# Optimization experiments

Hardware: AMD Instinct MI355X
Metric: run time of the kernel (lower is better)

The kernel has to match this reference:

```python
import jax, jax.numpy as jnp
import numpy as np

EMBED = 768
HEADS = 12
HEAD_DIM = EMBED // HEADS
HIDDEN = 4 * EMBED
EPS = 1e-5


def _layernorm(x, w, b):
    mu = jnp.mean(x, axis=-1, keepdims=True)
    var = jnp.mean(jnp.square(x - mu), axis=-1, keepdims=True)
    return (x - mu) * jax.lax.rsqrt(var + EPS) * w + b


def setup_inputs() -> dict:
    key = jax.random.key(0)
    ks = jax.random.split(key, 12)
    s = 0.02
    return {
        "x": jax.random.normal(ks[0], (2, 2048, EMBED), dtype=jnp.float32),
        "ln1_w": jnp.ones((EMBED,), jnp.float32),
        "ln1_b": jnp.zeros((EMBED,), jnp.float32),
        "qkv_w": jax.random.normal(ks[1], (3 * EMBED, EMBED), jnp.float32) * s,
        "qkv_b": jnp.zeros((3 * EMBED,), jnp.float32),
        "proj_w": jax.random.normal(ks[2], (EMBED, EMBED), jnp.float32) * s,
        "proj_b": jnp.zeros((EMBED,), jnp.float32),
        "ln2_w": jnp.ones((EMBED,), jnp.float32),
        "ln2_b": jnp.zeros((EMBED,), jnp.float32),
        "fc1_w": jax.random.normal(ks[3], (HIDDEN, EMBED), jnp.float32) * s,
        "fc1_b": jnp.zeros((HIDDEN,), jnp.float32),
        "fc2_w": jax.random.normal(ks[4], (EMBED, HIDDEN), jnp.float32) * s,
        "fc2_b": jnp.zeros((EMBED,), jnp.float32),
    }


def reference(x, ln1_w, ln1_b, qkv_w, qkv_b, proj_w, proj_b,
              ln2_w, ln2_b, fc1_w, fc1_b, fc2_w, fc2_b):
    B, N, C = x.shape
    scale = float(HEAD_DIM) ** 0.5  # NOTE: module MULTIPLIES by sqrt(head_dim)

    # --- attention branch ---
    h = _layernorm(x, ln1_w, ln1_b)
    qkv = h @ qkv_w.T + qkv_b                     # [B,N,3C]
    qkv = qkv.reshape(B, N, 3, HEADS, HEAD_DIM)
    q = qkv[:, :, 0].transpose(0, 2, 1, 3)        # [B,H,N,D]
    k = qkv[:, :, 1].transpose(0, 2, 1, 3)
    v = qkv[:, :, 2].transpose(0, 2, 1, 3)
    attn = jnp.einsum('bhnd,bhmd->bhnm', q, k) * scale
    attn = jax.nn.softmax(attn, axis=-1)
    o = jnp.einsum('bhnm,bhmd->bhnd', attn, v)    # [B,H,N,D]
    o = o.transpose(0, 2, 1, 3).reshape(B, N, C)
    x = x + (o @ proj_w.T + proj_b)

    # --- MLP branch ---
    h = _layernorm(x, ln2_w, ln2_b)
    h = jax.nn.gelu(h @ fc1_w.T + fc1_b, approximate=False)
    x = x + (h @ fc2_w.T + fc2_b)
    return x
```

## Files before the change

kernel.cpp:

```cpp
#include <hip/hip_runtime.h>
#include <hip/hip_bf16.h>

typedef __attribute__((ext_vector_type(8))) short short8;
typedef __attribute__((ext_vector_type(4))) float f32x4;
typedef __attribute__((ext_vector_type(4))) int i32x4;

__device__ inline unsigned short f2bs(float f) {
  union { float f; unsigned u; } v; v.f = f;
  unsigned r = v.u + 0x7fff + ((v.u >> 16) & 1);
  return (unsigned short)(r >> 16);
}

__device__ inline float bs2f(unsigned short u) {
  union { unsigned u; float f; } c; c.u = (unsigned)u << 16; return c.f;
}

__device__ inline unsigned pkbf(float a, float b) {
  __hip_bfloat162 h = __float22bfloat162_rn(float2{a, b});
  union { __hip_bfloat162 h; unsigned u; } c; c.h = h;
  return c.u;
}

__device__ inline float exp2v(float x) {
  float r; asm("v_exp_f32 %0, %1" : "=v"(r) : "v"(x)); return r;
}

__device__ inline float max3f(float a, float b, float c) {
  return fmaxf(fmaxf(a, b), c);
}

__device__ inline void gload16(const void* g, void* l) {
  __builtin_amdgcn_global_load_lds((const __attribute__((address_space(1))) void*)g,
                                   (__attribute__((address_space(3))) void*)l,
                                   16, 0, 0);
}

__global__ __launch_bounds__(256)
void cvt_all(const float* __restrict__ s0, const float* __restrict__ s1,
             const float* __restrict__ s2, const float* __restrict__ s3,
             unsigned short* __restrict__ d0, unsigned short* __restrict__ d1,
             unsigned short* __restrict__ d2, unsigned short* __restrict__ d3)
{
  size_t i = (size_t)blockIdx.x * 256 + threadIdx.x;
  const float* src; unsigned short* dst;
  if (i < 442368) { src = s0; dst = d0; }
  else if (i < 589824) { src = s1; dst = d1; i -= 442368; }
  else if (i < 1179648) { src = s2; dst = d2; i -= 589824; }
  else { src = s3; dst = d3; i -= 1179648; }
  float4 v = ((const float4*)src)[i];
  ushort4 o;
  o.x = f2bs(v.x); o.y = f2bs(v.y); o.z = f2bs(v.z); o.w = f2bs(v.w);
  ((ushort4*)dst)[i] = o;
}

__global__ __launch_bounds__(256)
void ln_kernel(const float* __restrict__ x, const float* __restrict__ w,
               const float* __restrict__ bsh, unsigned short* __restrict__ out)
{
  const int row = blockIdx.x;
  const float* xr = x + (size_t)row * 768;
  float v[3];
  float s = 0.f, sq = 0.f;
#pragma unroll
  for (int i = 0; i < 3; ++i) {
    v[i] = xr[threadIdx.x + i * 256];
    s += v[i]; sq += v[i] * v[i];
  }
#pragma unroll
  for (int d = 1; d < 64; d <<= 1) {
    s  += __shfl_xor(s, d, 64);
    sq += __shfl_xor(sq, d, 64);
  }
  __shared__ float ss[4], ssq[4];
  const int wv = threadIdx.x >> 6;
  if ((threadIdx.x & 63) == 0) { ss[wv] = s; ssq[wv] = sq; }
  __syncthreads();
  s  = ss[0] + ss[1] + ss[2] + ss[3];
  sq = ssq[0] + ssq[1] + ssq[2] + ssq[3];
  const float mu = s * (1.0f / 768.0f);
  const float var = sq * (1.0f / 768.0f) - mu * mu;
  const float rstd = rsqrtf(var + 1e-5f);
#pragma unroll
  for (int i = 0; i < 3; ++i) {
    const int c = threadIdx.x + i * 256;
    out[(size_t)row * 768 + c] = f2bs((v[i] - mu) * rstd * w[c] + bsh[c]);
  }
}

__global__ __launch_bounds__(256)
void reduce_ln2(const unsigned short* __restrict__ p, const float* __restrict__ bias,
                const float* __restrict__ resid, const float* __restrict__ lw,
                const float* __restrict__ lb, float* __restrict__ x2,
                unsigned short* __restrict__ h)
{
  const size_t MN = 4096ull * 768;
  const int row = blockIdx.x;
  const size_t r0 = (size_t)row * 768;
  float v[3];
  float s = 0.f, sq = 0.f;
#pragma unroll
  for (int i = 0; i < 3; ++i) {
    const int c = threadIdx.x + i * 256;
    const float a = bs2f(p[r0 + c]) + bs2f(p[MN + r0 + c]) + bias[c] + resid[r0 + c];
    x2[r0 + c] = a;
    v[i] = a; s += a; sq += a * a;
  }
#pragma unroll
  for (int d = 1; d < 64; d <<= 1) {
    s  += __shfl_xor(s, d, 64);
    sq += __shfl_xor(sq, d, 64);
  }
  __shared__ float ss[4], ssq[4];
  const int wv = threadIdx.x >> 6;
  if ((threadIdx.x & 63) == 0) { ss[wv] = s; ssq[wv] = sq; }
  __syncthreads();
  s  = ss[0] + ss[1] + ss[2] + ss[3];
  sq = ssq[0] + ssq[1] + ssq[2] + ssq[3];
  const float mu = s * (1.0f / 768.0f);
  const float var = sq * (1.0f / 768.0f) - mu * mu;
  const float rstd = rsqrtf(var + 1e-5f);
#pragma unroll
  for (int i = 0; i < 3; ++i) {
    const int c = threadIdx.x + i * 256;
    h[r0 + c] = f2bs((v[i] - mu) * rstd * lw[c] + lb[c]);
  }
}

template<int S>
__global__ __launch_bounds__(256)
void reduce_k(const unsigned short* __restrict__ p, const float* __restrict__ bias,
              const float* __restrict__ resid, float* __restrict__ out)
{
  const size_t MN = 4096ull * 768;
  const size_t i = ((size_t)blockIdx.x * 256 + threadIdx.x) * 4;
  float ax = 0.f, ay = 0.f, az = 0.f, aw = 0.f;
#pragma unroll
  for (int s = 0; s < S; ++s) {
    ushort4 b = *(const ushort4*)(p + s * MN + i);
    ax += bs2f(b.x); ay += bs2f(b.y); az += bs2f(b.z); aw += bs2f(b.w);
  }
  const int col = (int)(i % 768);
  float4 bb = *(const float4*)(bias + col);
  float4 rr = *(const float4*)(resid + i);
  float4 r;
  r.x = ax + bb.x + rr.x; r.y = ay + bb.y + rr.y;
  r.z = az + bb.z + rr.z; r.w = aw + bb.w + rr.w;
  *(float4*)(out + i) = r;
}

template<int EPI>
__global__ __launch_bounds__(256, 3)
void gemm_nt(const unsigned short* __restrict__ A,
             const unsigned short* __restrict__ Bw,
             const float* __restrict__ bias,
             const float* __restrict__ resid,
             void* __restrict__ out0, void* __restrict__ out1, void* __restrict__ out2,
             int M, int N, int Kslice, int Kstride)
{
  __shared__ __align__(16) unsigned short As[3][128 * 32];
  __shared__ __align__(16) unsigned short Bs[3][128 * 32];
  const int tid = threadIdx.x;
  const int lane = tid & 63;
  const int w = tid >> 6;
  const int wr = w >> 1, wc = w & 1;
  const int l15 = lane & 15, g = lane >> 4;

  const int nwg = gridDim.x * gridDim.y;
  const int hw = blockIdx.y * gridDim.x + blockIdx.x;
  const int virt = (hw & 7) * (nwg >> 3) + (hw >> 3);
  const int m0 = (virt / gridDim.x) * 128;
  const int n0 = (virt % gridDim.x) * 128;
  const int kbase = blockIdx.z * Kslice;

  f32x4 acc[4][4];
#pragma unroll
  for (int m = 0; m < 4; ++m)
#pragma unroll
    for (int n = 0; n < 4; ++n)
      acc[m][n] = (f32x4){0.f, 0.f, 0.f, 0.f};

  auto stage = [&](int buf, int k0) {
#pragma unroll
    for (int i = 0; i < 2; ++i) {
      const int f = tid + i * 256;
      const int row = f >> 2, c8 = f & 3;
      const int sc = c8 ^ (row & 3);
      gload16(A  + (size_t)(m0 + row) * Kstride + kbase + k0 + sc * 8, (char*)&As[buf][0] + f * 16);
      gload16(Bw + (size_t)(n0 + row) * Kstride + kbase + k0 + sc * 8, (char*)&Bs[buf][0] + f * 16);
    }
  };

  const int NT = Kslice >> 5;
  stage(0, 0);
  stage(1, 32);

  for (int t = 0; t < NT; ++t) {
    const int buf = t % 3;
    if (t + 1 < NT) {
      asm volatile("s_waitcnt vmcnt(4)" ::: "memory");
    } else {
      asm volatile("s_waitcnt vmcnt(0)" ::: "memory");
    }
    __builtin_amdgcn_s_barrier();
    asm volatile("" ::: "memory");
    if (t + 2 < NT) stage((t + 2) % 3, (t + 2) * 32);

    short8 af[4], bfr[4];
#pragma unroll
    for (int m = 0; m < 4; ++m) {
      const int r = wr * 64 + m * 16 + l15;
      af[m] = *(const short8*)((const char*)&As[buf][0] + ((size_t)r * 32 + (g ^ (r & 3)) * 8) * 2);
    }
#pragma unroll
    for (int n = 0; n < 4; ++n) {
      const int r = wc * 64 + n * 16 + l15;
      bfr[n] = *(const short8*)((const char*)&Bs[buf][0] + ((size_t)r * 32 + (g ^ (r & 3)) * 8) * 2);
    }
#pragma unroll
    for (int m = 0; m < 4; ++m)
#pragma unroll
      for (int n = 0; n < 4; ++n)
        acc[m][n] = __builtin_amdgcn_mfma_f32_16x16x32_bf16(af[m], bfr[n], acc[m][n], 0, 0, 0);
    asm volatile("" ::: "memory");
  }

#pragma unroll
  for (int m = 0; m < 4; ++m) {
    const int gmBase = m0 + wr * 64 + m * 16 + g * 4;
#pragma unroll
    for (int n = 0; n < 4; ++n) {
      const int gn = n0 + wc * 64 + n * 16 + l15;
      const float bval = (EPI == 4) ? 0.0f : bias[gn];
      float vj[4];
#pragma unroll
      for (int j = 0; j < 4; ++j) vj[j] = acc[m][n][j] + bval;
      if (EPI == 0) {
        const int three = gn / 768;
        const int hh = (gn % 768) >> 6;
        const int d = gn & 63;
        const int bb = gmBase >> 11, t = gmBase & 2047;
        if (three == 2) {
          ushort4 pk;
          pk.x = f2bs(vj[0]); pk.y = f2bs(vj[1]); pk.z = f2bs(vj[2]); pk.w = f2bs(vj[3]);
          const int kt = t & 63;
          const size_t pos = ((((size_t)(bb * 12 + hh) * 32 + (t >> 6)) * 8 + (d >> 4) * 2 + (kt >> 5)) * 64
                              + ((kt >> 2) & 3) * 16 + (d & 15)) * 8 + ((kt >> 4) & 1) * 4;
          *(ushort4*)((unsigned short*)out2 + pos) = pk;
        } else if (three == 1) {
          unsigned short* dst = (unsigned short*)out1;
          const int gt = t >> 6;
          const int kt0 = t & 63;
          const int fb = d >> 5;
          const int ge = (d >> 3) & 3;
          const int e = d & 7;
          const size_t base9 = ((size_t)(bb * 12 + hh) * 32 + gt) * 8;
#pragma unroll
          for (int j = 0; j < 4; ++j) {
            const int kt = kt0 + j;
            const size_t pos = (base9 + (kt >> 4) * 2 + fb) * 512 + (ge * 16 + (kt & 15)) * 8 + e;
            dst[pos] = f2bs(vj[j]);
          }
        } else {
          unsigned short* dst = (unsigned short*)out0;
#pragma unroll
          for (int j = 0; j < 4; ++j) {
            dst[(((size_t)bb * 12 + hh) * 2048 + (t + j)) * 64 + d] = f2bs(vj[j] * 11.5415603f);
          }
        }
      } else if (EPI == 1 || EPI == 3) {
#pragma unroll
        for (int j = 0; j < 4; ++j) {
          const int gm = gmBase + j;
          ((float*)out0)[(size_t)gm * N + gn] = vj[j] + resid[(size_t)gm * N + gn];
        }
      } else if (EPI == 2) {
#pragma unroll
        for (int j = 0; j < 4; ++j) {
          const int gm = gmBase + j;
          const float vv = vj[j];
          const float u = vv * (1.0f + 0.044715f * vv * vv);
          const float E = exp2v(2.0f * 0.7978845608f * 1.4426950409f * u);
          const float ge = vv - vv / (1.0f + E);
          ((unsigned short*)out0)[(size_t)gm * N + gn] = f2bs(ge);
        }
      } else {
        unsigned short* po = (unsigned short*)out0 + (size_t)blockIdx.z * M * N;
#pragma unroll
        for (int j = 0; j < 4; ++j) {
          const int gm = gmBase + j;
          po[(size_t)gm * N + gn] = f2bs(vj[j]);
        }
      }
    }
  }
}

template<int SPLIT>
__global__ __launch_bounds__(256, 6)
void attn_fwd(const unsigned short* __restrict__ Q,
              const unsigned short* __restrict__ Kf,
              const unsigned short* __restrict__ Vf,
              unsigned short* __restrict__ O,
              unsigned short* __restrict__ Op, float* __restrict__ Mb, float* __restrict__ Lb)
{
  __shared__ __align__(1024) unsigned short Ks[4096];
  __shared__ __align__(1024) unsigned short Vs[2][4096];
  const int tid = threadIdx.x, lane = tid & 63, w = tid >> 6;
  const int l15 = lane & 15, g = lane >> 4;

  const int hw = blockIdx.y * gridDim.x + blockIdx.x;
  const int virt = (hw & 7) * 96 + (hw >> 3);
  const int qblk = virt & 31;
  const int bh = virt >> 5;
  const int b = bh / 12, h = bh % 12;
  const int q0 = qblk * 64;
  const int half = SPLIT ? blockIdx.z : 0;
  const int NT = SPLIT ? 16 : 32;
  const int T0 = half * 16;
  const unsigned short* Qb = Q  + (size_t)bh * 2048 * 64;
  const unsigned short* Kb = Kf + (size_t)bh * 2048 * 64;
  const unsigned short* Vb = Vf + (size_t)bh * 2048 * 64;

  const int qr = q0 + w * 16 + l15;
  short8 qf[2];
  qf[0] = *(const short8*)(Qb + (size_t)qr * 64 + g * 8);
  qf[1] = *(const short8*)(Qb + (size_t)qr * 64 + 32 + g * 8);

  float m_run = -1e30f, l_part = 0.f;
  f32x4 o_acc[4];
#pragma unroll
  for (int dc = 0; dc < 4; ++dc) o_acc[dc] = (f32x4){0.f, 0.f, 0.f, 0.f};

  auto stageK = [&](int gt) {
#pragma unroll
    for (int i = 0; i < 2; ++i) {
      const int chunk = tid + i * 256;
      gload16(Kb + (size_t)gt * 4096 + chunk * 8, (char*)&Ks[0] + chunk * 16);
    }
  };
  auto stageV = [&](int buf, int gt) {
#pragma unroll
    for (int i = 0; i < 2; ++i) {
      const int chunk = tid + i * 256;
      gload16(Vb + (size_t)gt * 4096 + chunk * 8, (char*)&Vs[buf][0] + chunk * 16);
    }
  };

  stageK(T0);
  stageV(0, T0);

  for (int t = 0; t < NT; ++t) {
    const int vbuf = t & 1;
    asm volatile("s_waitcnt vmcnt(0)" ::: "memory");
    __builtin_amdgcn_s_barrier();
    asm volatile("" ::: "memory");
    if (t + 1 < NT) stageV(vbuf ^ 1, T0 + t + 1);

    f32x4 s2[4];
#pragma unroll
    for (int n = 0; n < 4; ++n) s2[n] = (f32x4){0.f, 0.f, 0.f, 0.f};
    __builtin_amdgcn_s_setprio(1);
#pragma unroll
    for (int n = 0; n < 4; ++n) {
      short8 kf0 = *(const short8*)(&Ks[(n * 2 + 0) * 512 + lane * 8]);
      short8 kf1 = *(const short8*)(&Ks[(n * 2 + 1) * 512 + lane * 8]);
      s2[n] = __builtin_amdgcn_mfma_f32_16x16x32_bf16(kf0, qf[0], s2[n], 0, 0, 0);
      s2[n] = __builtin_amdgcn_mfma_f32_16x16x32_bf16(kf1, qf[1], s2[n], 0, 0, 0);
    }
    __builtin_amdgcn_s_setprio(0);

    asm volatile("" ::: "memory");
    __builtin_amdgcn_s_barrier();
    asm volatile("" ::: "memory");
    if (t + 1 < NT) stageK(T0 + t + 1);

    float mx = max3f(max3f(s2[0][0], s2[0][1], s2[0][2]),
                     max3f(s2[0][3], s2[1][0], s2[1][1]),
                     max3f(s2[1][2], s2[1][3], s2[2][0]));
    mx = max3f(mx, max3f(s2[2][1], s2[2][2], s2[2][3]),
                   max3f(s2[3][0], s2[3][1], fmaxf(s2[3][2], s2[3][3])));
    mx = fmaxf(mx, __shfl_xor(mx, 16, 64));
    mx = fmaxf(mx, __shfl_xor(mx, 32, 64));
    if (__any(mx > m_run + 8.0f)) {
      const float mn = fmaxf(m_run, mx);
      const float alpha = exp2v(m_run - mn);
      m_run = mn;
      l_part *= alpha;
#pragma unroll
      for (int j = 0; j < 4; ++j) {
        const float aB = __shfl(alpha, (lane & 48) | (g * 4 + j), 64);
#pragma unroll
        for (int dc = 0; dc < 4; ++dc) o_acc[dc][j] *= aB;
      }
    }
    float e[4][4];
    float rs = 0.f;
#pragma unroll
    for (int n = 0; n < 4; ++n)
#pragma unroll
      for (int j = 0; j < 4; ++j) {
        e[n][j] = exp2v(s2[n][j] - m_run);
        rs += e[n][j];
      }
    l_part += rs;

    unsigned pw[2][4];
#pragma unroll
    for (int kc = 0; kc < 2; ++kc) {
      pw[kc][0] = pkbf(e[2 * kc][0],     e[2 * kc][1]);
      pw[kc][1] = pkbf(e[2 * kc][2],     e[2 * kc][3]);
      pw[kc][2] = pkbf(e[2 * kc + 1][0], e[2 * kc + 1][1]);
      pw[kc][3] = pkbf(e[2 * kc + 1][2], e[2 * kc + 1][3]);
    }

    const char* vsb = (const char*)&Vs[vbuf][0];
    __builtin_amdgcn_s_setprio(1);
#pragma unroll
    for (int kc = 0; kc < 2; ++kc) {
      i32x4 pt; pt.x = (int)pw[kc][0]; pt.y = (int)pw[kc][1]; pt.z = (int)pw[kc][2]; pt.w = (int)pw[kc][3];
      short8 pf = *(short8*)&pt;
#pragma unroll
      for (int dc = 0; dc < 4; ++dc) {
        short8 vfr = *(const short8*)(vsb + (((dc * 2 + kc) * 64 + lane) * 16));
        o_acc[dc] = __builtin_amdgcn_mfma_f32_16x16x32_bf16(pf, vfr, o_acc[dc], 0, 0, 0);
      }
    }
    __builtin_amdgcn_s_setprio(0);
    asm volatile("" ::: "memory");
  }

  l_part += __shfl_xor(l_part, 16, 64);
  l_part += __shfl_xor(l_part, 32, 64);
  if (SPLIT) {
    const int rowBase = (half * 24 + bh) * 2048;
    if (g == 0) {
      const int qm = q0 + w * 16 + l15;
      Mb[rowBase + qm] = m_run;
      Lb[rowBase + qm] = l_part;
    }
#pragma unroll
    for (int j = 0; j < 4; ++j) {
      const int row = q0 + w * 16 + g * 4 + j;
#pragma unroll
      for (int dc = 0; dc < 4; ++dc)
        Op[(size_t)(rowBase + row) * 64 + dc * 16 + l15] = f2bs(o_acc[dc][j]);
    }
  } else {
#pragma unroll
    for (int j = 0; j < 4; ++j) {
      const float lB = __shfl(l_part, (lane & 48) | (g * 4 + j), 64);
      const float inv = 1.0f / lB;
      const int qrow = q0 + w * 16 + g * 4 + j;
#pragma unroll
      for (int dc = 0; dc < 4; ++dc)
        O[((size_t)b * 2048 + qrow) * 768 + h * 64 + dc * 16 + l15] = f2bs(o_acc[dc][j] * inv);
    }
  }
}

__global__ __launch_bounds__(256)
void attn_combine(const unsigned short* __restrict__ Op, const float* __restrict__ Mb,
                  const float* __restrict__ Lb, unsigned short* __restrict__ O)
{
  const int idx = blockIdx.x * 256 + threadIdx.x;
  const int e4 = idx * 4;
  const int row = e4 >> 6;
  const int d0 = e4 & 63;
  const float m1 = Mb[row], m2 = Mb[49152 + row];
  const float l1 = Lb[row], l2 = Lb[49152 + row];
  const float mm = fmaxf(m1, m2);
  const float w1 = exp2v(m1 - mm), w2 = exp2v(m2 - mm);
  const float inv = 1.0f / (l1 * w1 + l2 * w2);
  ushort4 a1 = *(const ushort4*)(Op + (size_t)row * 64 + d0);
  ushort4 a2 = *(const ushort4*)(Op + 49152ull * 64 + (size_t)row * 64 + d0);
  ushort4 r;
  r.x = f2bs((bs2f(a1.x) * w1 + bs2f(a2.x) * w2) * inv);
  r.y = f2bs((bs2f(a1.y) * w1 + bs2f(a2.y) * w2) * inv);
  r.z = f2bs((bs2f(a1.z) * w1 + bs2f(a2.z) * w2) * inv);
  r.w = f2bs((bs2f(a1.w) * w1 + bs2f(a2.w) * w2) * inv);
  const int bh = row >> 11, q = row & 2047;
  const int b = bh / 12, hh = bh % 12;
  *(ushort4*)(O + ((size_t)(b * 2048 + q)) * 768 + hh * 64 + d0) = r;
}

extern "C" void kernel_launch(void* const* d_in, const int* in_sizes, int n_in,
                              void* d_out, int out_size, void* d_ws, size_t ws_size,
                              hipStream_t stream)
{
  const float* x      = (const float*)d_in[0];
  const float* ln1_w  = (const float*)d_in[1];
  const float* ln1_b  = (const float*)d_in[2];
  const float* qkv_w  = (const float*)d_in[3];
  const float* qkv_b  = (const float*)d_in[4];
  const float* proj_w = (const float*)d_in[5];
  const float* proj_b = (const float*)d_in[6];
  const float* ln2_w  = (const float*)d_in[7];
  const float* ln2_b  = (const float*)d_in[8];
  const float* fc1_w  = (const float*)d_in[9];
  const float* fc1_b  = (const float*)d_in[10];
  const float* fc2_w  = (const float*)d_in[11];
  const float* fc2_b  = (const float*)d_in[12];

  char* base = (char*)d_ws;
  size_t off = 0;
  auto take = [&](size_t bytes) {
    void* r = base + off;
    off = (off + bytes + 255) & ~(size_t)255;
    return r;
  };
  unsigned short* wq = (unsigned short*)take(2304ull * 768 * 2);
  unsigned short* wp = (unsigned short*)take(768ull * 768 * 2);
  unsigned short* w1 = (unsigned short*)take(3072ull * 768 * 2);
  unsigned short* w2 = (unsigned short*)take(768ull * 3072 * 2);
  unsigned short* h  = (unsigned short*)take(4096ull * 768 * 2);
  float* x2          = (float*)take(4096ull * 768 * 4);
  char* big          = (char*)take(4096ull * 3072 * 2);
  unsigned short* Qb = (unsigned short*)big;
  unsigned short* Kb = (unsigned short*)(big + 4096ull * 768 * 2);
  unsigned short* Vb = (unsigned short*)(big + 2ull * 4096 * 768 * 2);
  unsigned short* a2 = (unsigned short*)big;
  unsigned short* part = (unsigned short*)take(4ull * 4096 * 768 * 2);
  float* Mb_         = (float*)take(2ull * 49152 * 4);
  float* Lb_         = (float*)take(2ull * 49152 * 4);
  const bool can_split = off <= ws_size;

  cvt_all<<<6912, 256, 0, stream>>>(qkv_w, proj_w, fc1_w, fc2_w, wq, wp, w1, w2);

  ln_kernel<<<4096, 256, 0, stream>>>(x, ln1_w, ln1_b, h);
  gemm_nt<0><<<dim3(18, 32), 256, 0, stream>>>(h, wq, qkv_b, nullptr, Qb, Kb, Vb, 4096, 2304, 768, 768);

  if (can_split) {
    attn_fwd<1><<<dim3(32, 24, 2), 256, 0, stream>>>(Qb, Kb, Vb, nullptr, part, Mb_, Lb_);
    attn_combine<<<3072, 256, 0, stream>>>(part, Mb_, Lb_, h);
  } else {
    attn_fwd<0><<<dim3(32, 24), 256, 0, stream>>>(Qb, Kb, Vb, h, nullptr, nullptr, nullptr);
  }

  if (can_split) {
    gemm_nt<4><<<dim3(6, 32, 2), 256, 0, stream>>>(h, wp, nullptr, nullptr, part, nullptr, nullptr, 4096, 768, 384, 768);
    reduce_ln2<<<4096, 256, 0, stream>>>(part, proj_b, x, ln2_w, ln2_b, x2, h);
  } else {
    gemm_nt<1><<<dim3(6, 32), 256, 0, stream>>>(h, wp, proj_b, x, x2, nullptr, nullptr, 4096, 768, 768, 768);
    ln_kernel<<<4096, 256, 0, stream>>>(x2, ln2_w, ln2_b, h);
  }

  gemm_nt<2><<<dim3(24, 32), 256, 0, stream>>>(h, w1, fc1_b, nullptr, a2, nullptr, nullptr, 4096, 3072, 768, 768);

  if (can_split) {
    gemm_nt<4><<<dim3(6, 32, 4), 256, 0, stream>>>(a2, w2, nullptr, nullptr, part, nullptr, nullptr, 4096, 768, 768, 3072);
    reduce_k<4><<<3072, 256, 0, stream>>>(part, fc2_b, x2, (float*)d_out);
  } else {
    gemm_nt<3><<<dim3(6, 32), 256, 0, stream>>>(a2, w2, fc2_b, x2, d_out, nullptr, nullptr, 4096, 768, 3072, 3072);
  }
}
```

Before: 188.1 us.

## Process 128 query rows per attention block, split KV four ways, fuse prep

The attention kernel now has each wave handle two 16-row query groups (128 queries per block), so every K/V tile staged into LDS is reused by twice as many queries. The key range is split four ways instead of two, and the combine step merges four partial results. The weight conversion and first layernorm are merged into a single launch. This trades higher register pressure and a larger combine step for less LDS staging traffic and one fewer launch.

After: 241.9 us. 1.29x slower.

```diff
diff --git a/kernel.cpp b/kernel.cpp
--- a/kernel.cpp
+++ b/kernel.cpp
@@ -36,21 +36,54 @@
 }
 
 __global__ __launch_bounds__(256)
-void cvt_all(const float* __restrict__ s0, const float* __restrict__ s1,
-             const float* __restrict__ s2, const float* __restrict__ s3,
-             unsigned short* __restrict__ d0, unsigned short* __restrict__ d1,
-             unsigned short* __restrict__ d2, unsigned short* __restrict__ d3)
-{
-  size_t i = (size_t)blockIdx.x * 256 + threadIdx.x;
-  const float* src; unsigned short* dst;
-  if (i < 442368) { src = s0; dst = d0; }
-  else if (i < 589824) { src = s1; dst = d1; i -= 442368; }
-  else if (i < 1179648) { src = s2; dst = d2; i -= 589824; }
-  else { src = s3; dst = d3; i -= 1179648; }
-  float4 v = ((const float4*)src)[i];
-  ushort4 o;
-  o.x = f2bs(v.x); o.y = f2bs(v.y); o.z = f2bs(v.z); o.w = f2bs(v.w);
-  ((ushort4*)dst)[i] = o;
+void prep(const float* __restrict__ s0, const float* __restrict__ s1,
+          const float* __restrict__ s2, const float* __restrict__ s3,
+          unsigned short* __restrict__ d0, unsigned short* __restrict__ d1,
+          unsigned short* __restrict__ d2, unsigned short* __restrict__ d3,
+          const float* __restrict__ x, const float* __restrict__ lw,
+          const float* __restrict__ lb, unsigned short* __restrict__ out)
+{
+  if (blockIdx.x < 6912) {
+    size_t i = (size_t)blockIdx.x * 256 + threadIdx.x;
+    const float* src; unsigned short* dst;
+    if (i < 442368) { src = s0; dst = d0; }
+    else if (i < 589824) { src = s1; dst = d1; i -= 442368; }
+    else if (i < 1179648) { src = s2; dst = d2; i -= 589824; }
+    else { src = s3; dst = d3; i -= 1179648; }
+    float4 v = ((const float4*)src)[i];
+    ushort4 o;
+    o.x = f2bs(v.x); o.y = f2bs(v.y); o.z = f2bs(v.z); o.w = f2bs(v.w);
+    ((ushort4*)dst)[i] = o;
+    return;
+  }
+  const int row = blockIdx.x - 6912;
+  const float* xr = x + (size_t)row * 768;
+  float v[3];
+  float s = 0.f, sq = 0.f;
+#pragma unroll
+  for (int i = 0; i < 3; ++i) {
+    v[i] = xr[threadIdx.x + i * 256];
+    s += v[i]; sq += v[i] * v[i];
+  }
+#pragma unroll
+  for (int d = 1; d < 64; d <<= 1) {
+    s  += __shfl_xor(s, d, 64);
+    sq += __shfl_xor(sq, d, 64);
+  }
+  __shared__ float ss[4], ssq[4];
+  const int wv = threadIdx.x >> 6;
+  if ((threadIdx.x & 63) == 0) { ss[wv] = s; ssq[wv] = sq; }
+  __syncthreads();
+  s  = ss[0] + ss[1] + ss[2] + ss[3];
+  sq = ssq[0] + ssq[1] + ssq[2] + ssq[3];
+  const float mu = s * (1.0f / 768.0f);
+  const float var = sq * (1.0f / 768.0f) - mu * mu;
+  const float rstd = rsqrtf(var + 1e-5f);
+#pragma unroll
+  for (int i = 0; i < 3; ++i) {
+    const int c = threadIdx.x + i * 256;
+    out[(size_t)row * 768 + c] = f2bs((v[i] - mu) * rstd * lw[c] + lb[c]);
+  }
 }
 
 __global__ __launch_bounds__(256)
@@ -308,28 +341,32 @@
   const int tid = threadIdx.x, lane = tid & 63, w = tid >> 6;
   const int l15 = lane & 15, g = lane >> 4;
 
+  const int nwg = gridDim.x * gridDim.y;
   const int hw = blockIdx.y * gridDim.x + blockIdx.x;
-  const int virt = (hw & 7) * 96 + (hw >> 3);
-  const int qblk = virt & 31;
-  const int bh = virt >> 5;
+  const int virt = (hw & 7) * (nwg >> 3) + (hw >> 3);
+  const int qblk = virt & 15;
+  const int bh = virt >> 4;
   const int b = bh / 12, h = bh % 12;
-  const int q0 = qblk * 64;
-  const int half = SPLIT ? blockIdx.z : 0;
-  const int NT = SPLIT ? 16 : 32;
-  const int T0 = half * 16;
+  const int q0 = qblk * 128;
+  const int part = SPLIT ? blockIdx.z : 0;
+  const int NT = SPLIT ? 8 : 32;
+  const int T0 = part * 8;
   const unsigned short* Qb = Q  + (size_t)bh * 2048 * 64;
   const unsigned short* Kb = Kf + (size_t)bh * 2048 * 64;
   const unsigned short* Vb = Vf + (size_t)bh * 2048 * 64;
 
-  const int qr = q0 + w * 16 + l15;
-  short8 qf[2];
-  qf[0] = *(const short8*)(Qb + (size_t)qr * 64 + g * 8);
-  qf[1] = *(const short8*)(Qb + (size_t)qr * 64 + 32 + g * 8);
-
-  float m_run = -1e30f, l_part = 0.f;
-  f32x4 o_acc[4];
-#pragma unroll
-  for (int dc = 0; dc < 4; ++dc) o_acc[dc] = (f32x4){0.f, 0.f, 0.f, 0.f};
+  const int qra = q0 + w * 32 + l15;
+  const int qrb = qra + 16;
+  short8 qfa[2], qfb[2];
+  qfa[0] = *(const short8*)(Qb + (size_t)qra * 64 + g * 8);
+  qfa[1] = *(const short8*)(Qb + (size_t)qra * 64 + 32 + g * 8);
+  qfb[0] = *(const short8*)(Qb + (size_t)qrb * 64 + g * 8);
+  qfb[1] = *(const short8*)(Qb + (size_t)qrb * 64 + 32 + g * 8);
+
+  float m_a = -1e30f, l_a = 0.f, m_b = -1e30f, l_b = 0.f;
+  f32x4 oa[4], ob[4];
+#pragma unroll
+  for (int dc = 0; dc < 4; ++dc) { oa[dc] = (f32x4){0.f,0.f,0.f,0.f}; ob[dc] = (f32x4){0.f,0.f,0.f,0.f}; }
 
   auto stageK = [&](int gt) {
 #pragma unroll
@@ -364,8 +401,57 @@
     for (int n = 0; n < 4; ++n) {
       short8 kf0 = *(const short8*)(&Ks[(n * 2 + 0) * 512 + lane * 8]);
       short8 kf1 = *(const short8*)(&Ks[(n * 2 + 1) * 512 + lane * 8]);
-      s2[n] = __builtin_amdgcn_mfma_f32_16x16x32_bf16(kf0, qf[0], s2[n], 0, 0, 0);
-      s2[n] = __builtin_amdgcn_mfma_f32_16x16x32_bf16(kf1, qf[1], s2[n], 0, 0, 0);
+      s2[n] = __builtin_amdgcn_mfma_f32_16x16x32_bf16(kf0, qfa[0], s2[n], 0, 0, 0);
+      s2[n] = __builtin_amdgcn_mfma_f32_16x16x32_bf16(kf1, qfa[1], s2[n], 0, 0, 0);
+    }
+    __builtin_amdgcn_s_setprio(0);
+
+    unsigned pwa[2][4], pwb[2][4];
+    {
+      float mx = max3f(max3f(s2[0][0], s2[0][1], s2[0][2]),
+                       max3f(s2[0][3], s2[1][0], s2[1][1]),
+                       max3f(s2[1][2], s2[1][3], s2[2][0]));
+      mx = max3f(mx, max3f(s2[2][1], s2[2][2], s2[2][3]),
+                     max3f(s2[3][0], s2[3][1], fmaxf(s2[3][2], s2[3][3])));
+      mx = fmaxf(mx, __shfl_xor(mx, 16, 64));
+      mx = fmaxf(mx, __shfl_xor(mx, 32, 64));
+      if (__any(mx > m_a + 8.0f)) {
+        const float mn = fmaxf(m_a, mx);
+        const float alpha = exp2v(m_a - mn);
+        m_a = mn;
+        l_a *= alpha;
+#pragma unroll
+        for (int j = 0; j < 4; ++j) {
+          const float aB = __shfl(alpha, (lane & 48) | (g * 4 + j), 64);
+#pragma unroll
+          for (int dc = 0; dc < 4; ++dc) oa[dc][j] *= aB;
+        }
+      }
+      float rs = 0.f;
+#pragma unroll
+      for (int kc = 0; kc < 2; ++kc) {
+        float e0, e1;
+        e0 = exp2v(s2[2*kc][0] - m_a);   e1 = exp2v(s2[2*kc][1] - m_a);
+        rs += e0 + e1; pwa[kc][0] = pkbf(e0, e1);
+        e0 = exp2v(s2[2*kc][2] - m_a);   e1 = exp2v(s2[2*kc][3] - m_a);
+        rs += e0 + e1; pwa[kc][1] = pkbf(e0, e1);
+        e0 = exp2v(s2[2*kc+1][0] - m_a); e1 = exp2v(s2[2*kc+1][1] - m_a);
+        rs += e0 + e1; pwa[kc][2] = pkbf(e0, e1);
+        e0 = exp2v(s2[2*kc+1][2] - m_a); e1 = exp2v(s2[2*kc+1][3] - m_a);
+        rs += e0 + e1; pwa[kc][3] = pkbf(e0, e1);
+      }
+      l_a += rs;
+    }
+
+#pragma unroll
+    for (int n = 0; n < 4; ++n) s2[n] = (f32x4){0.f, 0.f, 0.f, 0.f};
+    __builtin_amdgcn_s_setprio(1);
+#pragma unroll
+    for (int n = 0; n < 4; ++n) {
+      short8 kf0 = *(const short8*)(&Ks[(n * 2 + 0) * 512 + lane * 8]);
+      short8 kf1 = *(const short8*)(&Ks[(n * 2 + 1) * 512 + lane * 8]);
+      s2[n] = __builtin_amdgcn_mfma_f32_16x16x32_bf16(kf0, qfb[0], s2[n], 0, 0, 0);
+      s2[n] = __builtin_amdgcn_mfma_f32_16x16x32_bf16(kf1, qfb[1], s2[n], 0, 0, 0);
     }
     __builtin_amdgcn_s_setprio(0);
 
@@ -374,86 +460,94 @@
     asm volatile("" ::: "memory");
     if (t + 1 < NT) stageK(T0 + t + 1);
 
-    float mx = max3f(max3f(s2[0][0], s2[0][1], s2[0][2]),
-                     max3f(s2[0][3], s2[1][0], s2[1][1]),
-                     max3f(s2[1][2], s2[1][3], s2[2][0]));
-    mx = max3f(mx, max3f(s2[2][1], s2[2][2], s2[2][3]),
-                   max3f(s2[3][0], s2[3][1], fmaxf(s2[3][2], s2[3][3])));
-    mx = fmaxf(mx, __shfl_xor(mx, 16, 64));
-    mx = fmaxf(mx, __shfl_xor(mx, 32, 64));
-    if (__any(mx > m_run + 8.0f)) {
-      const float mn = fmaxf(m_run, mx);
-      const float alpha = exp2v(m_run - mn);
-      m_run = mn;
-      l_part *= alpha;
-#pragma unroll
-      for (int j = 0; j < 4; ++j) {
-        const float aB = __shfl(alpha, (lane & 48) | (g * 4 + j), 64);
-#pragma unroll
-        for (int dc = 0; dc < 4; ++dc) o_acc[dc][j] *= aB;
-      }
-    }
-    float e[4][4];
-    float rs = 0.f;
-#pragma unroll
-    for (int n = 0; n < 4; ++n)
-#pragma unroll
-      for (int j = 0; j < 4; ++j) {
-        e[n][j] = exp2v(s2[n][j] - m_run);
-        rs += e[n][j];
-      }
-    l_part += rs;
-
-    unsigned pw[2][4];
-#pragma unroll
-    for (int kc = 0; kc < 2; ++kc) {
-      pw[kc][0] = pkbf(e[2 * kc][0],     e[2 * kc][1]);
-      pw[kc][1] = pkbf(e[2 * kc][2],     e[2 * kc][3]);
-      pw[kc][2] = pkbf(e[2 * kc + 1][0], e[2 * kc + 1][1]);
-      pw[kc][3] = pkbf(e[2 * kc + 1][2], e[2 * kc + 1][3]);
+    {
+      float mx = max3f(max3f(s2[0][0], s2[0][1], s2[0][2]),
+                       max3f(s2[0][3], s2[1][0], s2[1][1]),
+                       max3f(s2[1][2], s2[1][3], s2[2][0]));
+      mx = max3f(mx, max3f(s2[2][1], s2[2][2], s2[2][3]),
+                     max3f(s2[3][0], s2[3][1], fmaxf(s2[3][2], s2[3][3])));
+      mx = fmaxf(mx, __shfl_xor(mx, 16, 64));
+      mx = fmaxf(mx, __shfl_xor(mx, 32, 64));
+      if (__any(mx > m_b + 8.0f)) {
+        const float mn = fmaxf(m_b, mx);
+        const float alpha = exp2v(m_b - mn);
+        m_b = mn;
+        l_b *= alpha;
+#pragma unroll
+        for (int j = 0; j < 4; ++j) {
+          const float aB = __shfl(alpha, (lane & 48) | (g * 4 + j), 64);
+#pragma unroll
+          for (int dc = 0; dc < 4; ++dc) ob[dc][j] *= aB;
+        }
+      }
+      float rs = 0.f;
+#pragma unroll
+      for (int kc = 0; kc < 2; ++kc) {
+        float e0, e1;
+        e0 = exp2v(s2[2*kc][0] - m_b);   e1 = exp2v(s2[2*kc][1] - m_b);
+        rs += e0 + e1; pwb[kc][0] = pkbf(e0, e1);
+        e0 = exp2v(s2[2*kc][2] - m_b);   e1 = exp2v(s2[2*kc][3] - m_b);
+        rs += e0 + e1; pwb[kc][1] = pkbf(e0, e1);
+        e0 = exp2v(s2[2*kc+1][0] - m_b); e1 = exp2v(s2[2*kc+1][1] - m_b);
+        rs += e0 + e1; pwb[kc][2] = pkbf(e0, e1);
+        e0 = exp2v(s2[2*kc+1][2] - m_b); e1 = exp2v(s2[2*kc+1][3] - m_b);
+        rs += e0 + e1; pwb[kc][3] = pkbf(e0, e1);
+      }
+      l_b += rs;
     }
 
     const char* vsb = (const char*)&Vs[vbuf][0];
     __builtin_amdgcn_s_setprio(1);
 #pragma unroll
     for (int kc = 0; kc < 2; ++kc) {
-      i32x4 pt; pt.x = (int)pw[kc][0]; pt.y = (int)pw[kc][1]; pt.z = (int)pw[kc][2]; pt.w = (int)pw[kc][3];
-      short8 pf = *(short8*)&pt;
+      i32x4 pta; pta.x = (int)pwa[kc][0]; pta.y = (int)pwa[kc][1]; pta.z = (int)pwa[kc][2]; pta.w = (int)pwa[kc][3];
+      i32x4 ptb; ptb.x = (int)pwb[kc][0]; ptb.y = (int)pwb[kc][1]; ptb.z = (int)pwb[kc][2]; ptb.w = (int)pwb[kc][3];
+      short8 pfa = *(short8*)&pta;
+      short8 pfb = *(short8*)&ptb;
 #pragma unroll
       for (int dc = 0; dc < 4; ++dc) {
         short8 vfr = *(const short8*)(vsb + (((dc * 2 + kc) * 64 + lane) * 16));
-        o_acc[dc] = __builtin_amdgcn_mfma_f32_16x16x32_bf16(pf, vfr, o_acc[dc], 0, 0, 0);
+        oa[dc] = __builtin_amdgcn_mfma_f32_16x16x32_bf16(pfa, vfr, oa[dc], 0, 0, 0);
+        ob[dc] = __builtin_amdgcn_mfma_f32_16x16x32_bf16(pfb, vfr, ob[dc], 0, 0, 0);
       }
     }
     __builtin_amdgcn_s_setprio(0);
     asm volatile("" ::: "memory");
   }
 
-  l_part += __shfl_xor(l_part, 16, 64);
-  l_part += __shfl_xor(l_part, 32, 64);
+  l_a += __shfl_xor(l_a, 16, 64);
+  l_a += __shfl_xor(l_a, 32, 64);
+  l_b += __shfl_xor(l_b, 16, 64);
+  l_b += __shfl_xor(l_b, 32, 64);
   if (SPLIT) {
-    const int rowBase = (half * 24 + bh) * 2048;
+    const int rowBase = (part * 24 + bh) * 2048;
     if (g == 0) {
-      const int qm = q0 + w * 16 + l15;
-      Mb[rowBase + qm] = m_run;
-      Lb[rowBase + qm] = l_part;
+      Mb[rowBase + qra] = m_a;
+      Lb[rowBase + qra] = l_a;
+      Mb[rowBase + qrb] = m_b;
+      Lb[rowBase + qrb] = l_b;
     }
 #pragma unroll
     for (int j = 0; j < 4; ++j) {
-      const int row = q0 + w * 16 + g * 4 + j;
-#pragma unroll
-      for (int dc = 0; dc < 4; ++dc)
-        Op[(size_t)(rowBase + row) * 64 + dc * 16 + l15] = f2bs(o_acc[dc][j]);
+      const int rowA = q0 + w * 32 + g * 4 + j;
+#pragma unroll
+      for (int dc = 0; dc < 4; ++dc) {
+        Op[(size_t)(rowBase + rowA) * 64 + dc * 16 + l15] = f2bs(oa[dc][j]);
+        Op[(size_t)(rowBase + rowA + 16) * 64 + dc * 16 + l15] = f2bs(ob[dc][j]);
+      }
     }
   } else {
 #pragma unroll
     for (int j = 0; j < 4; ++j) {
-      const float lB = __shfl(l_part, (lane & 48) | (g * 4 + j), 64);
-      const float inv = 1.0f / lB;
-      const int qrow = q0 + w * 16 + g * 4 + j;
-#pragma unroll
-      for (int dc = 0; dc < 4; ++dc)
-        O[((size_t)b * 2048 + qrow) * 768 + h * 64 + dc * 16 + l15] = f2bs(o_acc[dc][j] * inv);
+      const int src = (lane & 48) | (g * 4 + j);
+      const float invA = 1.0f / __shfl(l_a, src, 64);
+      const float invB = 1.0f / __shfl(l_b, src, 64);
+      const int rowA = q0 + w * 32 + g * 4 + j;
+#pragma unroll
+      for (int dc = 0; dc < 4; ++dc) {
+        O[((size_t)b * 2048 + rowA) * 768 + h * 64 + dc * 16 + l15] = f2bs(oa[dc][j] * invA);
+        O[((size_t)b * 2048 + rowA + 16) * 768 + h * 64 + dc * 16 + l15] = f2bs(ob[dc][j] * invB);
+      }
     }
   }
 }
@@ -466,18 +560,20 @@
   const int e4 = idx * 4;
   const int row = e4 >> 6;
   const int d0 = e4 & 63;
-  const float m1 = Mb[row], m2 = Mb[49152 + row];
-  const float l1 = Lb[row], l2 = Lb[49152 + row];
-  const float mm = fmaxf(m1, m2);
-  const float w1 = exp2v(m1 - mm), w2 = exp2v(m2 - mm);
-  const float inv = 1.0f / (l1 * w1 + l2 * w2);
-  ushort4 a1 = *(const ushort4*)(Op + (size_t)row * 64 + d0);
-  ushort4 a2 = *(const ushort4*)(Op + 49152ull * 64 + (size_t)row * 64 + d0);
+  float m0 = Mb[row], m1 = Mb[49152 + row], m2 = Mb[2*49152 + row], m3 = Mb[3*49152 + row];
+  const float mm = fmaxf(fmaxf(m0, m1), fmaxf(m2, m3));
+  const float w0 = exp2v(m0 - mm), w1 = exp2v(m1 - mm), w2 = exp2v(m2 - mm), w3 = exp2v(m3 - mm);
+  const float inv = 1.0f / (Lb[row] * w0 + Lb[49152 + row] * w1 +
+                            Lb[2*49152 + row] * w2 + Lb[3*49152 + row] * w3);
+  ushort4 a0 = *(const ushort4*)(Op + (size_t)row * 64 + d0);
+  ushort4 a1 = *(const ushort4*)(Op + 49152ull * 64 + (size_t)row * 64 + d0);
+  ushort4 a2 = *(const ushort4*)(Op + 2ull * 49152 * 64 + (size_t)row * 64 + d0);
+  ushort4 a3 = *(const ushort4*)(Op + 3ull * 49152 * 64 + (size_t)row * 64 + d0);
   ushort4 r;
-  r.x = f2bs((bs2f(a1.x) * w1 + bs2f(a2.x) * w2) * inv);
-  r.y = f2bs((bs2f(a1.y) * w1 + bs2f(a2.y) * w2) * inv);
-  r.z = f2bs((bs2f(a1.z) * w1 + bs2f(a2.z) * w2) * inv);
-  r.w = f2bs((bs2f(a1.w) * w1 + bs2f(a2.w) * w2) * inv);
+  r.x = f2bs((bs2f(a0.x)*w0 + bs2f(a1.x)*w1 + bs2f(a2.x)*w2 + bs2f(a3.x)*w3) * inv);
+  r.y = f2bs((bs2f(a0.y)*w0 + bs2f(a1.y)*w1 + bs2f(a2.y)*w2 + bs2f(a3.y)*w3) * inv);
+  r.z = f2bs((bs2f(a0.z)*w0 + bs2f(a1.z)*w1 + bs2f(a2.z)*w2 + bs2f(a3.z)*w3) * inv);
+  r.w = f2bs((bs2f(a0.w)*w0 + bs2f(a1.w)*w1 + bs2f(a2.w)*w2 + bs2f(a3.w)*w3) * inv);
   const int bh = row >> 11, q = row & 2047;
   const int b = bh / 12, hh = bh % 12;
   *(ushort4*)(O + ((size_t)(b * 2048 + q)) * 768 + hh * 64 + d0) = r;
@@ -520,20 +616,19 @@
   unsigned short* Vb = (unsigned short*)(big + 2ull * 4096 * 768 * 2);
   unsigned short* a2 = (unsigned short*)big;
   unsigned short* part = (unsigned short*)take(4ull * 4096 * 768 * 2);
-  float* Mb_         = (float*)take(2ull * 49152 * 4);
-  float* Lb_         = (float*)take(2ull * 49152 * 4);
+  float* Mb_         = (float*)take(4ull * 49152 * 4);
+  float* Lb_         = (float*)take(4ull * 49152 * 4);
   const bool can_split = off <= ws_size;
 
-  cvt_all<<<6912, 256, 0, stream>>>(qkv_w, proj_w, fc1_w, fc2_w, wq, wp, w1, w2);
-
-  ln_kernel<<<4096, 256, 0, stream>>>(x, ln1_w, ln1_b, h);
+  prep<<<11008, 256, 0, stream>>>(qkv_w, proj_w, fc1_w, fc2_w, wq, wp, w1, w2,
+                                  x, ln1_w, ln1_b, h);
   gemm_nt<0><<<dim3(18, 32), 256, 0, stream>>>(h, wq, qkv_b, nullptr, Qb, Kb, Vb, 4096, 2304, 768, 768);
 
   if (can_split) {
-    attn_fwd<1><<<dim3(32, 24, 2), 256, 0, stream>>>(Qb, Kb, Vb, nullptr, part, Mb_, Lb_);
+    attn_fwd<1><<<dim3(16, 24, 4), 256, 0, stream>>>(Qb, Kb, Vb, nullptr, part, Mb_, Lb_);
     attn_combine<<<3072, 256, 0, stream>>>(part, Mb_, Lb_, h);
   } else {
-    attn_fwd<0><<<dim3(32, 24), 256, 0, stream>>>(Qb, Kb, Vb, h, nullptr, nullptr, nullptr);
+    attn_fwd<0><<<dim3(16, 24), 256, 0, stream>>>(Qb, Kb, Vb, h, nullptr, nullptr, nullptr);
   }
 
   if (can_split) {
```
